# Performance work log

Hardware: AMD Instinct MI355X
Metric: run time of the kernel (lower is better)

Reference implementation:

```python
import jax, jax.numpy as jnp
import numpy as np

HEADS = 8
DIM_HEAD = 64
SCALE = DIM_HEAD ** -0.5


def setup_inputs() -> dict:
    key = jax.random.key(0)
    ks = jax.random.split(key, 6)
    b, n, d = 2, 4096, 1024
    inner = HEADS * DIM_HEAD  # 512
    x = jax.random.normal(ks[0], (b, n, d), dtype=jnp.float32)
    Wq = jax.random.normal(ks[1], (d, inner), dtype=jnp.float32) * (d ** -0.5)
    Wk = jax.random.normal(ks[2], (d, inner), dtype=jnp.float32) * (d ** -0.5)
    Wv = jax.random.normal(ks[3], (d, inner), dtype=jnp.float32) * (d ** -0.5)
    Wout = jax.random.normal(ks[4], (inner, d), dtype=jnp.float32) * (inner ** -0.5)
    bout = jnp.zeros((d,), dtype=jnp.float32)
    return {"x": x, "Wq": Wq, "Wk": Wk, "Wv": Wv, "Wout": Wout, "bout": bout}


def reference(x, Wq, Wk, Wv, Wout, bout):
    b, n, _ = x.shape
    h, dh = HEADS, DIM_HEAD
    # self-attention: context = x
    q = (x @ Wq).reshape(b, n, h, dh).transpose(0, 2, 1, 3)  # b h n d
    k = (x @ Wk).reshape(b, n, h, dh).transpose(0, 2, 1, 3)
    v = (x @ Wv).reshape(b, n, h, dh).transpose(0, 2, 1, 3)
    sim = jnp.einsum('bhid,bhjd->bhij', q, k) * SCALE  # full score matrix
    attn = jax.nn.softmax(sim, axis=-1)
    out = jnp.einsum('bhij,bhjd->bhid', attn, v)
    out = out.transpose(0, 2, 1, 3).reshape(b, n, h * dh)  # b n (h d)
    return out @ Wout + bout
```

## Files before the change

kernel.cpp:

```cpp
#include <hip/hip_runtime.h>
#include <hip/hip_bf16.h>

typedef __bf16 bf16x8 __attribute__((ext_vector_type(8)));
typedef __bf16 bf16x4 __attribute__((ext_vector_type(4)));
typedef float floatx4 __attribute__((ext_vector_type(4)));

#define MFMA16(a, b, c) __builtin_amdgcn_mfma_f32_16x16x32_bf16((a), (b), (c), 0, 0, 0)

__device__ __forceinline__ void stage16(const __bf16* g, __bf16* lds_base) {
  __builtin_amdgcn_global_load_lds(
      (__attribute__((address_space(1))) void*)(void*)g,
      (__attribute__((address_space(3))) void*)lds_base, 16, 0, 0);
}

__global__ void detect_dtype(const unsigned int* __restrict__ x, int* __restrict__ flag) {
  __shared__ int cnt;
  if (threadIdx.x == 0) cnt = 0;
  __syncthreads();
  int c = 0;
  for (int i = threadIdx.x; i < 4096; i += 256) {
    const unsigned f = (x[i] >> 7) & 0xFF;
    c += (f >= 100 && f <= 140) ? 1 : 0;
  }
  atomicAdd(&cnt, c);
  __syncthreads();
  if (threadIdx.x == 0) *flag = (cnt > 2048) ? 1 : 0;
}

__global__ __launch_bounds__(256) void convert_x(const void* __restrict__ src,
                                                 __bf16* __restrict__ dst,
                                                 const int* __restrict__ flagp) {
  const int isbf = *flagp;
  const size_t i = ((size_t)blockIdx.x * 256 + threadIdx.x) * 8;
  if (isbf) {
    *(bf16x8*)(dst + i) = *(const bf16x8*)((const __bf16*)src + i);
  } else {
    const float4 f0 = *(const float4*)((const float*)src + i);
    const float4 f1 = *(const float4*)((const float*)src + i + 4);
    bf16x8 v;
    v[0] = (__bf16)f0.x; v[1] = (__bf16)f0.y; v[2] = (__bf16)f0.z; v[3] = (__bf16)f0.w;
    v[4] = (__bf16)f1.x; v[5] = (__bf16)f1.y; v[6] = (__bf16)f1.z; v[7] = (__bf16)f1.w;
    *(bf16x8*)(dst + i) = v;
  }
}

__global__ __launch_bounds__(256) void transpose3_conv(
    const void* __restrict__ s0, const void* __restrict__ s1,
    const void* __restrict__ s2, __bf16* __restrict__ dst,
    int R, int C, const int* __restrict__ flagp) {
  __shared__ __bf16 t[32][33];
  const int isbf = *flagp;
  const void* src = (blockIdx.z == 0) ? s0 : (blockIdx.z == 1) ? s1 : s2;
  __bf16* d = dst + (size_t)blockIdx.z * R * C;
  const int bx = blockIdx.x * 32, by = blockIdx.y * 32;
  const int x = threadIdx.x & 31, y0 = threadIdx.x >> 5;
#pragma unroll
  for (int i = y0; i < 32; i += 8) {
    const size_t idx = (size_t)(by + i) * C + bx + x;
    t[i][x] = isbf ? ((const __bf16*)src)[idx] : (__bf16)(((const float*)src)[idx]);
  }
  __syncthreads();
#pragma unroll
  for (int i = y0; i < 32; i += 8) d[(size_t)(bx + i) * R + by + x] = t[x][i];
}

__global__ __launch_bounds__(256) void transpose_conv(const void* __restrict__ src,
                                                      __bf16* __restrict__ dst,
                                                      int R, int C,
                                                      const int* __restrict__ flagp) {
  __shared__ __bf16 t[32][33];
  const int isbf = *flagp;
  const int bx = blockIdx.x * 32, by = blockIdx.y * 32;
  const int x = threadIdx.x & 31, y0 = threadIdx.x >> 5;
#pragma unroll
  for (int i = y0; i < 32; i += 8) {
    const size_t idx = (size_t)(by + i) * C + bx + x;
    t[i][x] = isbf ? ((const __bf16*)src)[idx] : (__bf16)(((const float*)src)[idx]);
  }
  __syncthreads();
#pragma unroll
  for (int i = y0; i < 32; i += 8) dst[(size_t)(bx + i) * R + by + x] = t[x][i];
}

__global__ __launch_bounds__(256) void vp_transpose(const __bf16* __restrict__ V,
                                                    __bf16* __restrict__ VP) {
  alignas(16) __shared__ __bf16 t[64][64];
  const int bh = blockIdx.y, s0 = blockIdx.x * 64;
  const int row = threadIdx.x >> 2, part = threadIdx.x & 3;
  const __bf16* src = V + (size_t)bh * 262144 + (size_t)(s0 + row) * 64 + part * 16;
  *(bf16x8*)&t[row][part * 16] = *(const bf16x8*)src;
  *(bf16x8*)&t[row][part * 16 + 8] = *(const bf16x8*)(src + 8);
  __syncthreads();
  const int d = row, og = part;
  bf16x8 w0, w1;
#pragma unroll
  for (int e = 0; e < 8; e++) {
    const int o0 = og * 16 + e, o1 = og * 16 + 8 + e;
    w0[e] = t[(o0 & 3) * 16 + (o0 >> 2)][d];
    w1[e] = t[(o1 & 3) * 16 + (o1 >> 2)][d];
  }
  __bf16* dst = VP + (size_t)bh * 262144 + (size_t)d * 4096 + s0 + og * 16;
  *(bf16x8*)dst = w0;
  *(bf16x8*)(dst + 8) = w1;
}

__global__ __launch_bounds__(256) void gemm_bt(
    const __bf16* __restrict__ A, const __bf16* __restrict__ Bt,
    void* __restrict__ Cv, void* __restrict__ Cv2, int M, int N, int K,
    const void* __restrict__ bias, int permute, int egress_dual,
    size_t zsB, size_t zsC, const int* __restrict__ flagp) {
  alignas(16) __shared__ __bf16 As[2][128 * 32];
  alignas(16) __shared__ __bf16 Bs[2][128 * 32];
  const int isbf = *flagp;
  Bt += blockIdx.z * zsB;
  const size_t zoff = (size_t)blockIdx.z * zsC;
  const int tid = threadIdx.x;
  const int wave = tid >> 6, lane = tid & 63;
  const int m0 = blockIdx.y * 128, n0 = blockIdx.x * 128;
  const int wm = (wave & 1) * 64, wn = (wave >> 1) * 64;
  const int fr = lane & 15, fq = lane >> 4;

  const floatx4 zero4 = {0.f, 0.f, 0.f, 0.f};
  floatx4 acc[4][4];
#pragma unroll
  for (int i = 0; i < 4; i++)
#pragma unroll
    for (int j = 0; j < 4; j++) acc[i][j] = zero4;

  const int lrow = lane >> 2;
  const int lk = (lane & 3) * 8;
  const int NT = K >> 5;

#pragma unroll
  for (int cc = 0; cc < 2; ++cc) {
    const int c = 2 * wave + cc;
    stage16(A + (size_t)(m0 + c * 16 + lrow) * K + lk, &As[0][c * 512]);
    stage16(Bt + (size_t)(n0 + c * 16 + lrow) * K + lk, &Bs[0][c * 512]);
  }

  for (int t = 0; t < NT; ++t) {
    const int cur = t & 1;
    if (t + 1 < NT) {
      const int k1 = (t + 1) << 5;
#pragma unroll
      for (int cc = 0; cc < 2; ++cc) {
        const int c = 2 * wave + cc;
        stage16(A + (size_t)(m0 + c * 16 + lrow) * K + k1 + lk, &As[1 - cur][c * 512]);
        stage16(Bt + (size_t)(n0 + c * 16 + lrow) * K + k1 + lk, &Bs[1 - cur][c * 512]);
      }
      asm volatile("s_waitcnt vmcnt(4)" ::: "memory");
    } else {
      asm volatile("s_waitcnt vmcnt(0)" ::: "memory");
    }
    __builtin_amdgcn_s_barrier();
    __builtin_amdgcn_sched_barrier(0);
    bf16x8 af[4], bg[4];
#pragma unroll
    for (int mt = 0; mt < 4; mt++)
      af[mt] = *(const bf16x8*)&As[cur][(wm + mt * 16 + fr) * 32 + fq * 8];
#pragma unroll
    for (int nt = 0; nt < 4; nt++)
      bg[nt] = *(const bf16x8*)&Bs[cur][(wn + nt * 16 + fr) * 32 + fq * 8];
#pragma unroll
    for (int mt = 0; mt < 4; mt++)
#pragma unroll
      for (int nt = 0; nt < 4; nt++)
        acc[mt][nt] = MFMA16(af[mt], bg[nt], acc[mt][nt]);
    __builtin_amdgcn_sched_barrier(0);
    __builtin_amdgcn_s_barrier();
  }

  const float qs = (permute && blockIdx.z == 0) ? 0.18033688011112042f
                                                : 1.0f;
#pragma unroll
  for (int mt = 0; mt < 4; mt++)
#pragma unroll
    for (int nt = 0; nt < 4; nt++)
#pragma unroll
      for (int r = 0; r < 4; r++) {
        const int row = m0 + wm + mt * 16 + fq * 4 + r;
        const int col = n0 + wn + nt * 16 + fr;
        float v = acc[mt][nt][r] * qs;
        if (bias)
          v += isbf ? (float)((const __bf16*)bias)[col] : ((const float*)bias)[col];
        if (permute) {
          const int bh = (row >> 12) * 8 + (col >> 6);
          const int s = row & 4095, d = col & 63;
          const size_t pidx = (size_t)bh * 262144 + (size_t)s * 64 + d;
          if (blockIdx.z == 2)
            ((__bf16*)Cv2)[pidx] = (__bf16)v;
          else
            ((__bf16*)Cv)[zoff + pidx] = (__bf16)v;
        } else {
          const size_t idx = (size_t)row * N + col;
          if (egress_dual && !isbf)
            ((float*)Cv)[idx] = v;
          else
            ((__bf16*)Cv)[idx] = (__bf16)v;
        }
      }
}

#define ATT_S 4096
__global__ __launch_bounds__(256, 2) void attn_flash(
    const __bf16* __restrict__ Qa, const __bf16* __restrict__ Ka,
    const __bf16* __restrict__ VPa, __bf16* __restrict__ O) {
  alignas(16) __shared__ __bf16 Kl[3][64 * 64];
  alignas(16) __shared__ __bf16 Vl[3][64 * 64];
  alignas(16) __shared__ __bf16 Pl[4 * 32 * 64];
  const int tid = threadIdx.x, wave = tid >> 6, lane = tid & 63;
  const int bh = blockIdx.y, b = bh >> 3, h = bh & 7;
  const int q0 = blockIdx.x * 128 + wave * 32;
  const int fr = lane & 15, fq = lane >> 4;
  const __bf16* Qb = Qa + (size_t)bh * ATT_S * 64;
  const __bf16* Kb = Ka + (size_t)bh * ATT_S * 64;
  const __bf16* Vb = VPa + (size_t)bh * ATT_S * 64;

  const int sw0 = ((fq ^ (fr & 7)) * 8);
  const int sw1 = (((fq + 4) ^ (fr & 7)) * 8);
  const int r0 = tid >> 3;
  const int ssw = (((tid & 7) ^ (r0 & 7)) * 8);

  bf16x8 aq[2][2];
#pragma unroll
  for (int mt = 0; mt < 2; mt++)
#pragma unroll
    for (int kt = 0; kt < 2; kt++)
      aq[mt][kt] = *(const bf16x8*)(Qb + (size_t)(q0 + mt * 16 + fr) * 64 + kt * 32 + fq * 8);

  const floatx4 zero4 = {0.f, 0.f, 0.f, 0.f};
  floatx4 o[2][4];
  float lsum[2][4];
#pragma unroll
  for (int mt = 0; mt < 2; mt++) {
#pragma unroll
    for (int nt = 0; nt < 4; nt++) o[mt][nt] = zero4;
#pragma unroll
    for (int r = 0; r < 4; r++) lsum[mt][r] = 0.f;
  }

  const int JT = ATT_S / 64;

#pragma unroll
  for (int t0 = 0; t0 < 2; ++t0) {
    const int kv = t0 * 64;
    stage16(Kb + (size_t)(kv + r0) * 64 + ssw, &Kl[t0][wave * 512]);
    stage16(Kb + (size_t)(kv + 32 + r0) * 64 + ssw, &Kl[t0][2048 + wave * 512]);
    stage16(Vb + (size_t)r0 * 4096 + kv + ssw, &Vl[t0][wave * 512]);
    stage16(Vb + (size_t)(32 + r0) * 4096 + kv + ssw, &Vl[t0][2048 + wave * 512]);
  }

  for (int j = 0; j < JT; ++j) {
    const int cur = j % 3;
    if (j + 2 < JT) {
      const int sl = (j + 2) % 3;
      const int kv2 = (j + 2) * 64;
      stage16(Kb + (size_t)(kv2 + r0) * 64 + ssw, &Kl[sl][wave * 512]);
      stage16(Kb + (size_t)(kv2 + 32 + r0) * 64 + ssw, &Kl[sl][2048 + wave * 512]);
      stage16(Vb + (size_t)r0 * 4096 + kv2 + ssw, &Vl[sl][wave * 512]);
      stage16(Vb + (size_t)(32 + r0) * 4096 + kv2 + ssw, &Vl[sl][2048 + wave * 512]);
      asm volatile("s_waitcnt vmcnt(8)" ::: "memory");
    } else if (j + 1 < JT) {
      asm volatile("s_waitcnt vmcnt(4)" ::: "memory");
    } else {
      asm volatile("s_waitcnt vmcnt(0)" ::: "memory");
    }
    __builtin_amdgcn_s_barrier();
    __builtin_amdgcn_sched_barrier(0);
    const __bf16* Klc = Kl[cur];
    const __bf16* Vlc = Vl[cur];

    floatx4 s4[2][4];
    __builtin_amdgcn_s_setprio(1);
#pragma unroll
    for (int nt = 0; nt < 4; nt++) {
      bf16x8 bk0 = *(const bf16x8*)&Klc[(nt * 16 + fr) * 64 + sw0];
      bf16x8 bk1 = *(const bf16x8*)&Klc[(nt * 16 + fr) * 64 + sw1];
#pragma unroll
      for (int mt = 0; mt < 2; mt++) {
        floatx4 zz = zero4;
        zz = MFMA16(aq[mt][0], bk0, zz);
        zz = MFMA16(aq[mt][1], bk1, zz);
        s4[mt][nt] = zz;
      }
    }
    __builtin_amdgcn_s_setprio(0);

#pragma unroll
    for (int mt = 0; mt < 2; mt++)
#pragma unroll
      for (int r = 0; r < 4; r++) {
        bf16x4 pv;
        float psum = 0.f;
#pragma unroll
        for (int nt = 0; nt < 4; nt++) {
          const float p = __builtin_amdgcn_exp2f(s4[mt][nt][r]);
          pv[nt] = (__bf16)p;
          psum += p;
        }
        lsum[mt][r] += psum;
        const int row = wave * 32 + mt * 16 + fq * 4 + r;
        const int vg = (fr >> 1) ^ ((fq * 4 + r) & 7);
        *(bf16x4*)&Pl[row * 64 + vg * 8 + (fr & 1) * 4] = pv;
      }
    asm volatile("s_waitcnt lgkmcnt(0)" ::: "memory");

    bf16x8 bv[4][2];
#pragma unroll
    for (int nt = 0; nt < 4; nt++) {
      bv[nt][0] = *(const bf16x8*)&Vlc[(nt * 16 + fr) * 64 + sw0];
      bv[nt][1] = *(const bf16x8*)&Vlc[(nt * 16 + fr) * 64 + sw1];
    }
    __builtin_amdgcn_s_setprio(1);
#pragma unroll
    for (int mt = 0; mt < 2; mt++) {
      const int prow = (wave * 32 + mt * 16 + fr) * 64;
      bf16x8 ap0 = *(const bf16x8*)&Pl[prow + sw0];
      bf16x8 ap1 = *(const bf16x8*)&Pl[prow + sw1];
#pragma unroll
      for (int nt = 0; nt < 4; nt++) {
        o[mt][nt] = MFMA16(ap0, bv[nt][0], o[mt][nt]);
        o[mt][nt] = MFMA16(ap1, bv[nt][1], o[mt][nt]);
      }
    }
    __builtin_amdgcn_s_setprio(0);
    __builtin_amdgcn_sched_barrier(0);
    __builtin_amdgcn_s_barrier();
  }

#pragma unroll
  for (int off = 1; off < 16; off <<= 1)
#pragma unroll
    for (int mt = 0; mt < 2; mt++)
#pragma unroll
      for (int r = 0; r < 4; r++) lsum[mt][r] += __shfl_xor(lsum[mt][r], off, 64);

#pragma unroll
  for (int mt = 0; mt < 2; mt++)
#pragma unroll
    for (int r = 0; r < 4; r++) {
      const float inv = 1.0f / lsum[mt][r];
      const int row = q0 + mt * 16 + fq * 4 + r;
      __bf16* Orow = O + (size_t)(b * ATT_S + row) * 512 + h * 64;
#pragma unroll
      for (int nt = 0; nt < 4; nt++)
        Orow[nt * 16 + fr] = (__bf16)(o[mt][nt][r] * inv);
    }
}

extern "C" void kernel_launch(void* const* d_in, const int* in_sizes, int n_in,
                              void* d_out, int out_size, void* d_ws, size_t ws_size,
                              hipStream_t stream) {
  (void)in_sizes; (void)n_in; (void)out_size; (void)ws_size;
  const void* x = d_in[0];
  const void* Wq = d_in[1];
  const void* Wk = d_in[2];
  const void* Wv = d_in[3];
  const void* Wout = d_in[4];
  const void* bout = d_in[5];

  char* ws = (char*)d_ws;
  int* flag = (int*)ws;
  __bf16* wtq = (__bf16*)(ws + (1u << 20));
  __bf16* wto = (__bf16*)(ws + (4u << 20));
  __bf16* Q = (__bf16*)(ws + (5u << 20));
  __bf16* K = (__bf16*)(ws + (13u << 20));
  __bf16* VP = (__bf16*)(ws + (21u << 20));
  __bf16* O = (__bf16*)(ws + (29u << 20));
  __bf16* Vtmp = O;
  __bf16* xbf = (__bf16*)(ws + (38u << 20));

  detect_dtype<<<1, 256, 0, stream>>>((const unsigned int*)x, flag);

  transpose3_conv<<<dim3(16, 32, 3), 256, 0, stream>>>(Wq, Wk, Wv, wtq, 1024, 512, flag);
  transpose_conv<<<dim3(32, 16), 256, 0, stream>>>(Wout, wto, 512, 1024, flag);

  convert_x<<<4096, 256, 0, stream>>>(x, xbf, flag);

  gemm_bt<<<dim3(4, 64, 3), 256, 0, stream>>>(
      xbf, wtq, Q, Vtmp, 8192, 512, 1024, nullptr, 1, 0,
      (size_t)512 * 1024, (size_t)8192 * 512, flag);

  vp_transpose<<<dim3(64, 16), 256, 0, stream>>>(Vtmp, VP);

  attn_flash<<<dim3(ATT_S / 128, 16), 256, 0, stream>>>(Q, K, VP, O);

  gemm_bt<<<dim3(8, 64, 1), 256, 0, stream>>>(
      O, wto, d_out, nullptr, 8192, 1024, 512, bout, 0, 1, 0, 0, flag);
}
```

Measured before the change: 260.6 us.

## Fuse QKV GEMM into one N=1536 launch and swizzle workgroups across XCDs

The three z-sliced QKV projection GEMMs become a single GEMM with N=1536, which relies on wtq holding the three transposed weights contiguously. The epilogue derives the plane and q-scale from the column index. Both the GEMMs and the attention kernel remap block IDs with a stride-8 swizzle, so that blocks sharing A rows or the same head land on the same XCD and reuse its L2. The remap assumes the grid sizes are divisible by 8 and that the attention grid is exactly 32x16.

```diff
diff --git a/kernel.cpp b/kernel.cpp
--- a/kernel.cpp
+++ b/kernel.cpp
@@ -108,15 +108,20 @@
     const __bf16* __restrict__ A, const __bf16* __restrict__ Bt,
     void* __restrict__ Cv, void* __restrict__ Cv2, int M, int N, int K,
     const void* __restrict__ bias, int permute, int egress_dual,
-    size_t zsB, size_t zsC, const int* __restrict__ flagp) {
+    size_t zsC, const int* __restrict__ flagp) {
   alignas(16) __shared__ __bf16 As[2][128 * 32];
   alignas(16) __shared__ __bf16 Bs[2][128 * 32];
   const int isbf = *flagp;
-  Bt += blockIdx.z * zsB;
-  const size_t zoff = (size_t)blockIdx.z * zsC;
+  const int gx = gridDim.x;
+  const int nwg = gx * gridDim.y;
+  const int orig = blockIdx.x + blockIdx.y * gx;
+  const int qq = nwg >> 3;
+  const int swz = (orig & 7) * qq + (orig >> 3);
+  const int bx = swz % gx, by = swz / gx;
+
   const int tid = threadIdx.x;
   const int wave = tid >> 6, lane = tid & 63;
-  const int m0 = blockIdx.y * 128, n0 = blockIdx.x * 128;
+  const int m0 = by * 128, n0 = bx * 128;
   const int wm = (wave & 1) * 64, wn = (wave >> 1) * 64;
   const int fr = lane & 15, fq = lane >> 4;
 
@@ -170,8 +175,8 @@
     __builtin_amdgcn_s_barrier();
   }
 
-  const float qs = (permute && blockIdx.z == 0) ? 0.18033688011112042f
-                                                : 1.0f;
+  const float qs = (permute && n0 < 512) ? 0.18033688011112042f
+                                         : 1.0f;
 #pragma unroll
   for (int mt = 0; mt < 4; mt++)
 #pragma unroll
@@ -184,13 +189,15 @@
         if (bias)
           v += isbf ? (float)((const __bf16*)bias)[col] : ((const float*)bias)[col];
         if (permute) {
-          const int bh = (row >> 12) * 8 + (col >> 6);
+          const int plane = col >> 9;
+          const int pc = col & 511;
+          const int bh = ((row >> 12) << 3) + (pc >> 6);
           const int s = row & 4095, d = col & 63;
           const size_t pidx = (size_t)bh * 262144 + (size_t)s * 64 + d;
-          if (blockIdx.z == 2)
+          if (plane == 2)
             ((__bf16*)Cv2)[pidx] = (__bf16)v;
           else
-            ((__bf16*)Cv)[zoff + pidx] = (__bf16)v;
+            ((__bf16*)Cv)[(size_t)plane * zsC + pidx] = (__bf16)v;
         } else {
           const size_t idx = (size_t)row * N + col;
           if (egress_dual && !isbf)
@@ -209,8 +216,11 @@
   alignas(16) __shared__ __bf16 Vl[3][64 * 64];
   alignas(16) __shared__ __bf16 Pl[4 * 32 * 64];
   const int tid = threadIdx.x, wave = tid >> 6, lane = tid & 63;
-  const int bh = blockIdx.y, b = bh >> 3, h = bh & 7;
-  const int q0 = blockIdx.x * 128 + wave * 32;
+  const int orig = blockIdx.x + blockIdx.y * 32;
+  const int swz = (orig & 7) * 64 + (orig >> 3);
+  const int qx = swz & 31, bh = swz >> 5;
+  const int b = bh >> 3, h = bh & 7;
+  const int q0 = qx * 128 + wave * 32;
   const int fr = lane & 15, fq = lane >> 4;
   const __bf16* Qb = Qa + (size_t)bh * ATT_S * 64;
   const __bf16* Kb = Ka + (size_t)bh * ATT_S * 64;
@@ -377,14 +387,14 @@
 
   convert_x<<<4096, 256, 0, stream>>>(x, xbf, flag);
 
-  gemm_bt<<<dim3(4, 64, 3), 256, 0, stream>>>(
-      xbf, wtq, Q, Vtmp, 8192, 512, 1024, nullptr, 1, 0,
-      (size_t)512 * 1024, (size_t)8192 * 512, flag);
+  gemm_bt<<<dim3(12, 64, 1), 256, 0, stream>>>(
+      xbf, wtq, Q, Vtmp, 8192, 1536, 1024, nullptr, 1, 0,
+      (size_t)8192 * 512, flag);
 
   vp_transpose<<<dim3(64, 16), 256, 0, stream>>>(Vtmp, VP);
 
   attn_flash<<<dim3(ATT_S / 128, 16), 256, 0, stream>>>(Q, K, VP, O);
 
   gemm_bt<<<dim3(8, 64, 1), 256, 0, stream>>>(
-      O, wto, d_out, nullptr, 8192, 1024, 512, bout, 0, 1, 0, 0, flag);
-}
+      O, wto, d_out, nullptr, 8192, 1024, 512, bout, 0, 1, 0, flag);
+}
```

Measured after the change: 254.0 us. 1.03x faster.
